# Optimization experiments

Measured on AMD Instinct MI355X. Metric: run time of the kernel, lower is better.

## Reference

```python
import jax, jax.numpy as jnp
import numpy as np

GRAVITY, MAIN_THRUST, SIDE_TORQUE, DT = 10.0, 6.0, 1.0, 0.02
H_OBS = jnp.array([[1, 0, 0, 0, 0, 0],
                   [0, 1, 0, 0, 0, 0],
                   [0, 0, 0, 0, 1, 0]], dtype=jnp.float32)  # (3,6)


def build_psd(log_diag, off_diag, dim):
    rows, cols = np.tril_indices(dim, -1)  # row-major, same order as torch.tril_indices
    L = jnp.zeros((dim, dim), dtype=log_diag.dtype)
    L = L.at[jnp.arange(dim), jnp.arange(dim)].set(jnp.exp(log_diag))
    L = L.at[rows, cols].set(off_diag)
    return L @ L.T + 1e-6 * jnp.eye(dim, dtype=log_diag.dtype)


def setup_inputs() -> dict:
    key = jax.random.key(0)
    B = 524288
    ks = jax.random.split(key, 8)
    z = jax.random.normal(ks[0], (B, 3), dtype=jnp.float32)
    u = jax.random.uniform(ks[1], (B, 2), dtype=jnp.float32)
    x_prev = jax.random.normal(ks[2], (B, 6), dtype=jnp.float32)
    A = 0.1 * jax.random.normal(ks[3], (B, 6, 6), dtype=jnp.float32)
    P_prev = jnp.einsum('bij,bkj->bik', A, A) + 0.5 * jnp.eye(6, dtype=jnp.float32)
    q_log_diag = jnp.array([-3.0, -3.0, -2.0, -2.0, -3.0, -2.0], dtype=jnp.float32)
    q_off_diag = 0.01 * jax.random.normal(ks[4], (15,), dtype=jnp.float32)
    r_log_diag = jnp.array([-2.0, -2.0, -2.0], dtype=jnp.float32)
    r_off_diag = 0.01 * jax.random.normal(ks[5], (3,), dtype=jnp.float32)
    return {"z": z, "u": u, "x_prev": x_prev, "P_prev": P_prev,
            "q_log_diag": q_log_diag, "q_off_diag": q_off_diag,
            "r_log_diag": r_log_diag, "r_off_diag": r_off_diag}


def _dynamics(x, u):
    px, py, vx, vy, theta, omega = (x[:, i] for i in range(6))
    main_power = jnp.clip(u[:, 0], 0.0, 1.0)
    lateral = u[:, 1]
    sin_th, cos_th = jnp.sin(theta), jnp.cos(theta)
    ax = -MAIN_THRUST * sin_th * main_power
    ay = MAIN_THRUST * cos_th * main_power - GRAVITY
    alpha = SIDE_TORQUE * lateral
    new_vx = vx + ax * DT
    new_vy = vy + ay * DT
    new_omega = omega + alpha * DT
    new_px = px + new_vx * DT
    new_py = py + new_vy * DT
    new_theta = theta + new_omega * DT
    return jnp.stack([new_px, new_py, new_vx, new_vy, new_theta, new_omega], axis=-1)


def _dynamics_jacobian(x, u):
    B = x.shape[0]
    theta = x[:, 4]
    main_power = jnp.clip(u[:, 0], 0.0, 1.0)
    sin_th, cos_th = jnp.sin(theta), jnp.cos(theta)
    Tm = MAIN_THRUST * main_power
    d = jnp.arange(6)
    F = jnp.zeros((B, 6, 6), dtype=x.dtype).at[:, d, d].set(1.0)
    F = F.at[:, 0, 2].set(DT).at[:, 1, 3].set(DT).at[:, 4, 5].set(DT)
    F = F.at[:, 2, 4].set(-Tm * cos_th * DT)
    F = F.at[:, 3, 4].set(-Tm * sin_th * DT)
    F = F.at[:, 0, 4].set(-Tm * cos_th * (DT * DT))
    F = F.at[:, 1, 4].set(-Tm * sin_th * (DT * DT))
    return F


def reference(z, u, x_prev, P_prev, q_log_diag, q_off_diag, r_log_diag, r_off_diag):
    Q = build_psd(q_log_diag, q_off_diag, 6)
    R = build_psd(r_log_diag, r_off_diag, 3)
    H = H_OBS
    # predict
    x_pred = _dynamics(x_prev, u)                              # (B,6)
    F = _dynamics_jacobian(x_prev, u)                          # (B,6,6)
    P_pred = jnp.einsum('bij,bjk,blk->bil', F, P_prev, F) + Q  # F P F^T + Q
    # update
    z_pred = jnp.einsum('ij,bj->bi', H, x_pred)                # (B,3)
    y = z - z_pred
    HP = jnp.einsum('ij,bjk->bik', H, P_pred)                  # (B,3,6)
    S = jnp.einsum('bij,kj->bik', HP, H) + R                   # (B,3,3)
    K = jnp.swapaxes(jnp.linalg.solve(S, HP), -1, -2)          # (B,6,3)
    x_upd = x_pred + jnp.einsum('bij,bj->bi', K, y)
    IKH = jnp.eye(6, dtype=x_pred.dtype) - jnp.einsum('bij,jk->bik', K, H)
    P_upd = (jnp.einsum('bij,bjk,blk->bil', IKH, P_pred, IKH)
             + jnp.einsum('bij,jk,blk->bil', K, R, K))          # Joseph form
    return (x_upd, P_upd)
```

## Files before the change

kernel.cpp:

```cpp
#include <hip/hip_runtime.h>

namespace {
constexpr float GRAVITY     = 10.0f;
constexpr float MAIN_THRUST = 6.0f;
constexpr float DT          = 0.02f;
}

__global__ __launch_bounds__(256) void ekf_kernel(
    const float* __restrict__ z,
    const float* __restrict__ u,
    const float* __restrict__ x_prev,
    const float* __restrict__ P_prev,
    const float* __restrict__ q_log_diag,
    const float* __restrict__ q_off_diag,
    const float* __restrict__ r_log_diag,
    const float* __restrict__ r_off_diag,
    float* __restrict__ x_out,
    float* __restrict__ P_out,
    int B)
{
    const int b = blockIdx.x * blockDim.x + threadIdx.x;
    if (b >= B) return;

    float L[6][6];
    #pragma unroll
    for (int i = 0; i < 6; ++i)
        #pragma unroll
        for (int j = 0; j < 6; ++j) L[i][j] = 0.0f;
    #pragma unroll
    for (int i = 0; i < 6; ++i) L[i][i] = expf(q_log_diag[i]);
    L[1][0] = q_off_diag[0];
    L[2][0] = q_off_diag[1];  L[2][1] = q_off_diag[2];
    L[3][0] = q_off_diag[3];  L[3][1] = q_off_diag[4];  L[3][2] = q_off_diag[5];
    L[4][0] = q_off_diag[6];  L[4][1] = q_off_diag[7];  L[4][2] = q_off_diag[8];
    L[4][3] = q_off_diag[9];
    L[5][0] = q_off_diag[10]; L[5][1] = q_off_diag[11]; L[5][2] = q_off_diag[12];
    L[5][3] = q_off_diag[13]; L[5][4] = q_off_diag[14];

    float Q[6][6];
    #pragma unroll
    for (int i = 0; i < 6; ++i) {
        #pragma unroll
        for (int j = 0; j <= i; ++j) {
            float s = 0.0f;
            #pragma unroll
            for (int k = 0; k <= j; ++k) s += L[i][k] * L[j][k];
            if (i == j) s += 1e-6f;
            Q[i][j] = s;
            Q[j][i] = s;
        }
    }

    float rd0 = expf(r_log_diag[0]);
    float rd1 = expf(r_log_diag[1]);
    float rd2 = expf(r_log_diag[2]);
    float ro0 = r_off_diag[0], ro1 = r_off_diag[1], ro2 = r_off_diag[2];
    float R00 = rd0 * rd0 + 1e-6f;
    float R10 = ro0 * rd0;
    float R11 = ro0 * ro0 + rd1 * rd1 + 1e-6f;
    float R20 = ro1 * rd0;
    float R21 = ro1 * ro0 + ro2 * rd1;
    float R22 = ro1 * ro1 + ro2 * ro2 + rd2 * rd2 + 1e-6f;
    float Rm[3][3] = {{R00, R10, R20}, {R10, R11, R21}, {R20, R21, R22}};

    const float2* xp2 = reinterpret_cast<const float2*>(x_prev + 6 * b);
    float2 x01 = xp2[0], x23 = xp2[1], x45 = xp2[2];
    const float px = x01.x, py = x01.y, vx = x23.x, vy = x23.y;
    const float th = x45.x, om = x45.y;

    const float2 uu = *reinterpret_cast<const float2*>(u + 2 * b);
    const float mp  = fminf(fmaxf(uu.x, 0.0f), 1.0f);
    const float lat = uu.y;

    float s_th, c_th;
    __sincosf(th, &s_th, &c_th);

    const float Tm  = MAIN_THRUST * mp;
    const float ax  = -Tm * s_th;
    const float ay  =  Tm * c_th - GRAVITY;
    const float nvx = vx + ax * DT;
    const float nvy = vy + ay * DT;
    const float nom = om + lat * DT;
    const float npx = px + nvx * DT;
    const float npy = py + nvy * DT;
    const float nth = th + nom * DT;
    float xp[6] = {npx, npy, nvx, nvy, nth, nom};

    const float f24 = -Tm * c_th * DT;
    const float f34 = -Tm * s_th * DT;
    const float f04 = f24 * DT;
    const float f14 = f34 * DT;

    float P[36];
    const float4* Pp4 = reinterpret_cast<const float4*>(P_prev + 36 * b);
    #pragma unroll
    for (int i = 0; i < 9; ++i) {
        float4 v = Pp4[i];
        P[4 * i + 0] = v.x; P[4 * i + 1] = v.y;
        P[4 * i + 2] = v.z; P[4 * i + 3] = v.w;
    }

    #pragma unroll
    for (int j = 0; j < 6; ++j) {
        P[0 * 6 + j] += DT * P[2 * 6 + j] + f04 * P[4 * 6 + j];
        P[1 * 6 + j] += DT * P[3 * 6 + j] + f14 * P[4 * 6 + j];
        P[2 * 6 + j] += f24 * P[4 * 6 + j];
        P[3 * 6 + j] += f34 * P[4 * 6 + j];
        P[4 * 6 + j] += DT * P[5 * 6 + j];
    }
    #pragma unroll
    for (int i = 0; i < 6; ++i) {
        const float m0 = P[i * 6 + 0], m1 = P[i * 6 + 1], m2 = P[i * 6 + 2];
        const float m3 = P[i * 6 + 3], m4 = P[i * 6 + 4], m5 = P[i * 6 + 5];
        P[i * 6 + 0] = m0 + DT * m2 + f04 * m4 + Q[i][0];
        P[i * 6 + 1] = m1 + DT * m3 + f14 * m4 + Q[i][1];
        P[i * 6 + 2] = m2 + f24 * m4 + Q[i][2];
        P[i * 6 + 3] = m3 + f34 * m4 + Q[i][3];
        P[i * 6 + 4] = m4 + DT * m5 + Q[i][4];
        P[i * 6 + 5] = m5 + Q[i][5];
    }

    const float* zp = z + 3 * b;
    const float y0 = zp[0] - npx;
    const float y1 = zp[1] - npy;
    const float y2 = zp[2] - nth;

    const float s00 = P[0 * 6 + 0] + Rm[0][0];
    const float s01 = P[0 * 6 + 1] + Rm[0][1];
    const float s02 = P[0 * 6 + 4] + Rm[0][2];
    const float s10 = P[1 * 6 + 0] + Rm[1][0];
    const float s11 = P[1 * 6 + 1] + Rm[1][1];
    const float s12 = P[1 * 6 + 4] + Rm[1][2];
    const float s20 = P[4 * 6 + 0] + Rm[2][0];
    const float s21 = P[4 * 6 + 1] + Rm[2][1];
    const float s22 = P[4 * 6 + 4] + Rm[2][2];

    const float det = s00 * (s11 * s22 - s12 * s21)
                    + s01 * (s12 * s20 - s10 * s22)
                    + s02 * (s10 * s21 - s11 * s20);
    const float invd = 1.0f / det;
    const float i00 = (s11 * s22 - s12 * s21) * invd;
    const float i01 = (s02 * s21 - s01 * s22) * invd;
    const float i02 = (s01 * s12 - s02 * s11) * invd;
    const float i10 = (s12 * s20 - s10 * s22) * invd;
    const float i11 = (s00 * s22 - s02 * s20) * invd;
    const float i12 = (s02 * s10 - s00 * s12) * invd;
    const float i20 = (s10 * s21 - s11 * s20) * invd;
    const float i21 = (s01 * s20 - s00 * s21) * invd;
    const float i22 = (s00 * s11 - s01 * s10) * invd;

    float K[6][3];
    #pragma unroll
    for (int i = 0; i < 6; ++i) {
        const float hp0 = P[0 * 6 + i];
        const float hp1 = P[1 * 6 + i];
        const float hp2 = P[4 * 6 + i];
        K[i][0] = i00 * hp0 + i01 * hp1 + i02 * hp2;
        K[i][1] = i10 * hp0 + i11 * hp1 + i12 * hp2;
        K[i][2] = i20 * hp0 + i21 * hp1 + i22 * hp2;
    }

    float2* xo2 = reinterpret_cast<float2*>(x_out + 6 * b);
    float xu[6];
    #pragma unroll
    for (int i = 0; i < 6; ++i)
        xu[i] = xp[i] + K[i][0] * y0 + K[i][1] * y1 + K[i][2] * y2;
    xo2[0] = make_float2(xu[0], xu[1]);
    xo2[1] = make_float2(xu[2], xu[3]);
    xo2[2] = make_float2(xu[4], xu[5]);

    float r0[6], r1[6], r4[6];
    #pragma unroll
    for (int j = 0; j < 6; ++j) {
        r0[j] = P[0 * 6 + j];
        r1[j] = P[1 * 6 + j];
        r4[j] = P[4 * 6 + j];
    }
    #pragma unroll
    for (int i = 0; i < 6; ++i)
        #pragma unroll
        for (int j = 0; j < 6; ++j)
            P[i * 6 + j] -= K[i][0] * r0[j] + K[i][1] * r1[j] + K[i][2] * r4[j];

    float c0[6], c1[6], c4[6];
    #pragma unroll
    for (int i = 0; i < 6; ++i) {
        c0[i] = P[i * 6 + 0];
        c1[i] = P[i * 6 + 1];
        c4[i] = P[i * 6 + 4];
    }
    float KR[6][3];
    #pragma unroll
    for (int i = 0; i < 6; ++i) {
        #pragma unroll
        for (int a = 0; a < 3; ++a)
            KR[i][a] = K[i][0] * Rm[0][a] + K[i][1] * Rm[1][a] + K[i][2] * Rm[2][a];
    }
    #pragma unroll
    for (int i = 0; i < 6; ++i) {
        #pragma unroll
        for (int j = 0; j < 6; ++j) {
            P[i * 6 + j] += -(c0[i] * K[j][0] + c1[i] * K[j][1] + c4[i] * K[j][2])
                            + (KR[i][0] * K[j][0] + KR[i][1] * K[j][1] + KR[i][2] * K[j][2]);
        }
    }

    float4* Po4 = reinterpret_cast<float4*>(P_out + 36 * b);
    #pragma unroll
    for (int i = 0; i < 9; ++i) {
        float4 v;
        v.x = P[4 * i + 0]; v.y = P[4 * i + 1];
        v.z = P[4 * i + 2]; v.w = P[4 * i + 3];
        Po4[i] = v;
    }
}

extern "C" void kernel_launch(void* const* d_in, const int* in_sizes, int n_in,
                              void* d_out, int out_size, void* d_ws, size_t ws_size,
                              hipStream_t stream) {
    const float* z          = (const float*)d_in[0];
    const float* u          = (const float*)d_in[1];
    const float* x_prev     = (const float*)d_in[2];
    const float* P_prev     = (const float*)d_in[3];
    const float* q_log_diag = (const float*)d_in[4];
    const float* q_off_diag = (const float*)d_in[5];
    const float* r_log_diag = (const float*)d_in[6];
    const float* r_off_diag = (const float*)d_in[7];

    const int B = in_sizes[0] / 3;
    float* x_out = (float*)d_out;
    float* P_out = (float*)d_out + (size_t)B * 6;

    const int block = 256;
    const int grid  = (B + block - 1) / block;
    ekf_kernel<<<grid, block, 0, stream>>>(z, u, x_prev, P_prev,
                                           q_log_diag, q_off_diag,
                                           r_log_diag, r_off_diag,
                                           x_out, P_out, B);
}
```

Before: 196.1 us.

## Stage P covariance loads and stores through padded shared memory for coalescing

Each block now loads its P_prev tile into shared memory with block-wide coalesced float4 reads, and threads read their own row from a stride-37 padded layout meant to avoid bank conflicts. After computing, each thread writes its result row back to shared memory, and the block writes P_out with coalesced float4 stores. This targets the strided per-thread 144-byte accesses of the old version. In exchange it adds about 37 KB of shared memory per block, which may limit occupancy, plus two barriers.

```diff
diff --git a/kernel.cpp b/kernel.cpp
--- a/kernel.cpp
+++ b/kernel.cpp
@@ -4,9 +4,11 @@
 constexpr float GRAVITY     = 10.0f;
 constexpr float MAIN_THRUST = 6.0f;
 constexpr float DT          = 0.02f;
+constexpr int   BLK         = 256;
+constexpr int   ROWPAD      = 37;
 }
 
-__global__ __launch_bounds__(256) void ekf_kernel(
+__global__ __launch_bounds__(BLK) void ekf_kernel(
     const float* __restrict__ z,
     const float* __restrict__ u,
     const float* __restrict__ x_prev,
@@ -19,199 +21,233 @@
     float* __restrict__ P_out,
     int B)
 {
-    const int b = blockIdx.x * blockDim.x + threadIdx.x;
-    if (b >= B) return;
-
-    float L[6][6];
-    #pragma unroll
-    for (int i = 0; i < 6; ++i)
-        #pragma unroll
-        for (int j = 0; j < 6; ++j) L[i][j] = 0.0f;
-    #pragma unroll
-    for (int i = 0; i < 6; ++i) L[i][i] = expf(q_log_diag[i]);
-    L[1][0] = q_off_diag[0];
-    L[2][0] = q_off_diag[1];  L[2][1] = q_off_diag[2];
-    L[3][0] = q_off_diag[3];  L[3][1] = q_off_diag[4];  L[3][2] = q_off_diag[5];
-    L[4][0] = q_off_diag[6];  L[4][1] = q_off_diag[7];  L[4][2] = q_off_diag[8];
-    L[4][3] = q_off_diag[9];
-    L[5][0] = q_off_diag[10]; L[5][1] = q_off_diag[11]; L[5][2] = q_off_diag[12];
-    L[5][3] = q_off_diag[13]; L[5][4] = q_off_diag[14];
-
-    float Q[6][6];
-    #pragma unroll
-    for (int i = 0; i < 6; ++i) {
-        #pragma unroll
-        for (int j = 0; j <= i; ++j) {
-            float s = 0.0f;
-            #pragma unroll
-            for (int k = 0; k <= j; ++k) s += L[i][k] * L[j][k];
-            if (i == j) s += 1e-6f;
-            Q[i][j] = s;
-            Q[j][i] = s;
+    __shared__ float smem[BLK * ROWPAD];
+
+    const int t = threadIdx.x;
+    const long long blockElem0 = (long long)blockIdx.x * BLK;
+    const long long elemsLeft  = (long long)B - blockElem0;
+    const int nElem  = elemsLeft >= BLK ? BLK : (int)elemsLeft;
+    const int count4 = nElem * 9;
+
+    {
+        const float4* gP4 = reinterpret_cast<const float4*>(P_prev + blockElem0 * 36);
+        #pragma unroll
+        for (int k = 0; k < 9; ++k) {
+            const int g4 = t + k * BLK;
+            if (g4 < count4) {
+                const float4 v = gP4[g4];
+                const int elem = g4 / 9;
+                const int off4 = g4 % 9;
+                float* dst = &smem[elem * ROWPAD + off4 * 4];
+                dst[0] = v.x; dst[1] = v.y; dst[2] = v.z; dst[3] = v.w;
+            }
         }
     }
-
-    float rd0 = expf(r_log_diag[0]);
-    float rd1 = expf(r_log_diag[1]);
-    float rd2 = expf(r_log_diag[2]);
-    float ro0 = r_off_diag[0], ro1 = r_off_diag[1], ro2 = r_off_diag[2];
-    float R00 = rd0 * rd0 + 1e-6f;
-    float R10 = ro0 * rd0;
-    float R11 = ro0 * ro0 + rd1 * rd1 + 1e-6f;
-    float R20 = ro1 * rd0;
-    float R21 = ro1 * ro0 + ro2 * rd1;
-    float R22 = ro1 * ro1 + ro2 * ro2 + rd2 * rd2 + 1e-6f;
-    float Rm[3][3] = {{R00, R10, R20}, {R10, R11, R21}, {R20, R21, R22}};
-
-    const float2* xp2 = reinterpret_cast<const float2*>(x_prev + 6 * b);
-    float2 x01 = xp2[0], x23 = xp2[1], x45 = xp2[2];
-    const float px = x01.x, py = x01.y, vx = x23.x, vy = x23.y;
-    const float th = x45.x, om = x45.y;
-
-    const float2 uu = *reinterpret_cast<const float2*>(u + 2 * b);
-    const float mp  = fminf(fmaxf(uu.x, 0.0f), 1.0f);
-    const float lat = uu.y;
-
-    float s_th, c_th;
-    __sincosf(th, &s_th, &c_th);
-
-    const float Tm  = MAIN_THRUST * mp;
-    const float ax  = -Tm * s_th;
-    const float ay  =  Tm * c_th - GRAVITY;
-    const float nvx = vx + ax * DT;
-    const float nvy = vy + ay * DT;
-    const float nom = om + lat * DT;
-    const float npx = px + nvx * DT;
-    const float npy = py + nvy * DT;
-    const float nth = th + nom * DT;
-    float xp[6] = {npx, npy, nvx, nvy, nth, nom};
-
-    const float f24 = -Tm * c_th * DT;
-    const float f34 = -Tm * s_th * DT;
-    const float f04 = f24 * DT;
-    const float f14 = f34 * DT;
-
-    float P[36];
-    const float4* Pp4 = reinterpret_cast<const float4*>(P_prev + 36 * b);
-    #pragma unroll
-    for (int i = 0; i < 9; ++i) {
-        float4 v = Pp4[i];
-        P[4 * i + 0] = v.x; P[4 * i + 1] = v.y;
-        P[4 * i + 2] = v.z; P[4 * i + 3] = v.w;
+    __syncthreads();
+
+    const bool valid = (t < nElem);
+    const long long b = blockElem0 + t;
+
+    if (valid) {
+        float L[6][6];
+        #pragma unroll
+        for (int i = 0; i < 6; ++i)
+            #pragma unroll
+            for (int j = 0; j < 6; ++j) L[i][j] = 0.0f;
+        #pragma unroll
+        for (int i = 0; i < 6; ++i) L[i][i] = expf(q_log_diag[i]);
+        L[1][0] = q_off_diag[0];
+        L[2][0] = q_off_diag[1];  L[2][1] = q_off_diag[2];
+        L[3][0] = q_off_diag[3];  L[3][1] = q_off_diag[4];  L[3][2] = q_off_diag[5];
+        L[4][0] = q_off_diag[6];  L[4][1] = q_off_diag[7];  L[4][2] = q_off_diag[8];
+        L[4][3] = q_off_diag[9];
+        L[5][0] = q_off_diag[10]; L[5][1] = q_off_diag[11]; L[5][2] = q_off_diag[12];
+        L[5][3] = q_off_diag[13]; L[5][4] = q_off_diag[14];
+
+        float Q[6][6];
+        #pragma unroll
+        for (int i = 0; i < 6; ++i) {
+            #pragma unroll
+            for (int j = 0; j <= i; ++j) {
+                float s = 0.0f;
+                #pragma unroll
+                for (int k = 0; k <= j; ++k) s += L[i][k] * L[j][k];
+                if (i == j) s += 1e-6f;
+                Q[i][j] = s;
+                Q[j][i] = s;
+            }
+        }
+
+        const float rd0 = expf(r_log_diag[0]);
+        const float rd1 = expf(r_log_diag[1]);
+        const float rd2 = expf(r_log_diag[2]);
+        const float ro0 = r_off_diag[0], ro1 = r_off_diag[1], ro2 = r_off_diag[2];
+        const float R00 = rd0 * rd0 + 1e-6f;
+        const float R10 = ro0 * rd0;
+        const float R11 = ro0 * ro0 + rd1 * rd1 + 1e-6f;
+        const float R20 = ro1 * rd0;
+        const float R21 = ro1 * ro0 + ro2 * rd1;
+        const float R22 = ro1 * ro1 + ro2 * ro2 + rd2 * rd2 + 1e-6f;
+        const float Rm[3][3] = {{R00, R10, R20}, {R10, R11, R21}, {R20, R21, R22}};
+
+        const float2* xp2 = reinterpret_cast<const float2*>(x_prev + 6 * b);
+        const float2 x01 = xp2[0], x23 = xp2[1], x45 = xp2[2];
+        const float px = x01.x, py = x01.y, vx = x23.x, vy = x23.y;
+        const float th = x45.x, om = x45.y;
+
+        const float2 uu = *reinterpret_cast<const float2*>(u + 2 * b);
+        const float mp  = fminf(fmaxf(uu.x, 0.0f), 1.0f);
+        const float lat = uu.y;
+
+        float s_th, c_th;
+        __sincosf(th, &s_th, &c_th);
+
+        const float Tm  = MAIN_THRUST * mp;
+        const float ax  = -Tm * s_th;
+        const float ay  =  Tm * c_th - GRAVITY;
+        const float nvx = vx + ax * DT;
+        const float nvy = vy + ay * DT;
+        const float nom = om + lat * DT;
+        const float npx = px + nvx * DT;
+        const float npy = py + nvy * DT;
+        const float nth = th + nom * DT;
+        const float xp[6] = {npx, npy, nvx, nvy, nth, nom};
+
+        const float f24 = -Tm * c_th * DT;
+        const float f34 = -Tm * s_th * DT;
+        const float f04 = f24 * DT;
+        const float f14 = f34 * DT;
+
+        float P[36];
+        const float* myrow = &smem[t * ROWPAD];
+        #pragma unroll
+        for (int j = 0; j < 36; ++j) P[j] = myrow[j];
+
+        #pragma unroll
+        for (int j = 0; j < 6; ++j) {
+            P[0 * 6 + j] += DT * P[2 * 6 + j] + f04 * P[4 * 6 + j];
+            P[1 * 6 + j] += DT * P[3 * 6 + j] + f14 * P[4 * 6 + j];
+            P[2 * 6 + j] += f24 * P[4 * 6 + j];
+            P[3 * 6 + j] += f34 * P[4 * 6 + j];
+            P[4 * 6 + j] += DT * P[5 * 6 + j];
+        }
+        #pragma unroll
+        for (int i = 0; i < 6; ++i) {
+            const float m0 = P[i * 6 + 0], m1 = P[i * 6 + 1], m2 = P[i * 6 + 2];
+            const float m3 = P[i * 6 + 3], m4 = P[i * 6 + 4], m5 = P[i * 6 + 5];
+            P[i * 6 + 0] = m0 + DT * m2 + f04 * m4 + Q[i][0];
+            P[i * 6 + 1] = m1 + DT * m3 + f14 * m4 + Q[i][1];
+            P[i * 6 + 2] = m2 + f24 * m4 + Q[i][2];
+            P[i * 6 + 3] = m3 + f34 * m4 + Q[i][3];
+            P[i * 6 + 4] = m4 + DT * m5 + Q[i][4];
+            P[i * 6 + 5] = m5 + Q[i][5];
+        }
+
+        const float* zp = z + 3 * b;
+        const float y0 = zp[0] - npx;
+        const float y1 = zp[1] - npy;
+        const float y2 = zp[2] - nth;
+
+        const float s00 = P[0 * 6 + 0] + Rm[0][0];
+        const float s01 = P[0 * 6 + 1] + Rm[0][1];
+        const float s02 = P[0 * 6 + 4] + Rm[0][2];
+        const float s10 = P[1 * 6 + 0] + Rm[1][0];
+        const float s11 = P[1 * 6 + 1] + Rm[1][1];
+        const float s12 = P[1 * 6 + 4] + Rm[1][2];
+        const float s20 = P[4 * 6 + 0] + Rm[2][0];
+        const float s21 = P[4 * 6 + 1] + Rm[2][1];
+        const float s22 = P[4 * 6 + 4] + Rm[2][2];
+
+        const float det = s00 * (s11 * s22 - s12 * s21)
+                        + s01 * (s12 * s20 - s10 * s22)
+                        + s02 * (s10 * s21 - s11 * s20);
+        const float invd = 1.0f / det;
+        const float i00 = (s11 * s22 - s12 * s21) * invd;
+        const float i01 = (s02 * s21 - s01 * s22) * invd;
+        const float i02 = (s01 * s12 - s02 * s11) * invd;
+        const float i10 = (s12 * s20 - s10 * s22) * invd;
+        const float i11 = (s00 * s22 - s02 * s20) * invd;
+        const float i12 = (s02 * s10 - s00 * s12) * invd;
+        const float i20 = (s10 * s21 - s11 * s20) * invd;
+        const float i21 = (s01 * s20 - s00 * s21) * invd;
+        const float i22 = (s00 * s11 - s01 * s10) * invd;
+
+        float K[6][3];
+        #pragma unroll
+        for (int i = 0; i < 6; ++i) {
+            const float hp0 = P[0 * 6 + i];
+            const float hp1 = P[1 * 6 + i];
+            const float hp2 = P[4 * 6 + i];
+            K[i][0] = i00 * hp0 + i01 * hp1 + i02 * hp2;
+            K[i][1] = i10 * hp0 + i11 * hp1 + i12 * hp2;
+            K[i][2] = i20 * hp0 + i21 * hp1 + i22 * hp2;
+        }
+
+        float2* xo2 = reinterpret_cast<float2*>(x_out + 6 * b);
+        float xu[6];
+        #pragma unroll
+        for (int i = 0; i < 6; ++i)
+            xu[i] = xp[i] + K[i][0] * y0 + K[i][1] * y1 + K[i][2] * y2;
+        xo2[0] = make_float2(xu[0], xu[1]);
+        xo2[1] = make_float2(xu[2], xu[3]);
+        xo2[2] = make_float2(xu[4], xu[5]);
+
+        float r0[6], r1[6], r4[6];
+        #pragma unroll
+        for (int j = 0; j < 6; ++j) {
+            r0[j] = P[0 * 6 + j];
+            r1[j] = P[1 * 6 + j];
+            r4[j] = P[4 * 6 + j];
+        }
+        #pragma unroll
+        for (int i = 0; i < 6; ++i)
+            #pragma unroll
+            for (int j = 0; j < 6; ++j)
+                P[i * 6 + j] -= K[i][0] * r0[j] + K[i][1] * r1[j] + K[i][2] * r4[j];
+
+        float c0[6], c1[6], c4[6];
+        #pragma unroll
+        for (int i = 0; i < 6; ++i) {
+            c0[i] = P[i * 6 + 0];
+            c1[i] = P[i * 6 + 1];
+            c4[i] = P[i * 6 + 4];
+        }
+        float KR[6][3];
+        #pragma unroll
+        for (int i = 0; i < 6; ++i) {
+            #pragma unroll
+            for (int a = 0; a < 3; ++a)
+                KR[i][a] = K[i][0] * Rm[0][a] + K[i][1] * Rm[1][a] + K[i][2] * Rm[2][a];
+        }
+        #pragma unroll
+        for (int i = 0; i < 6; ++i) {
+            #pragma unroll
+            for (int j = 0; j < 6; ++j) {
+                P[i * 6 + j] += -(c0[i] * K[j][0] + c1[i] * K[j][1] + c4[i] * K[j][2])
+                                + (KR[i][0] * K[j][0] + KR[i][1] * K[j][1] + KR[i][2] * K[j][2]);
+            }
+        }
+
+        float* myrowW = &smem[t * ROWPAD];
+        #pragma unroll
+        for (int j = 0; j < 36; ++j) myrowW[j] = P[j];
     }
-
-    #pragma unroll
-    for (int j = 0; j < 6; ++j) {
-        P[0 * 6 + j] += DT * P[2 * 6 + j] + f04 * P[4 * 6 + j];
-        P[1 * 6 + j] += DT * P[3 * 6 + j] + f14 * P[4 * 6 + j];
-        P[2 * 6 + j] += f24 * P[4 * 6 + j];
-        P[3 * 6 + j] += f34 * P[4 * 6 + j];
-        P[4 * 6 + j] += DT * P[5 * 6 + j];
-    }
-    #pragma unroll
-    for (int i = 0; i < 6; ++i) {
-        const float m0 = P[i * 6 + 0], m1 = P[i * 6 + 1], m2 = P[i * 6 + 2];
-        const float m3 = P[i * 6 + 3], m4 = P[i * 6 + 4], m5 = P[i * 6 + 5];
-        P[i * 6 + 0] = m0 + DT * m2 + f04 * m4 + Q[i][0];
-        P[i * 6 + 1] = m1 + DT * m3 + f14 * m4 + Q[i][1];
-        P[i * 6 + 2] = m2 + f24 * m4 + Q[i][2];
-        P[i * 6 + 3] = m3 + f34 * m4 + Q[i][3];
-        P[i * 6 + 4] = m4 + DT * m5 + Q[i][4];
-        P[i * 6 + 5] = m5 + Q[i][5];
-    }
-
-    const float* zp = z + 3 * b;
-    const float y0 = zp[0] - npx;
-    const float y1 = zp[1] - npy;
-    const float y2 = zp[2] - nth;
-
-    const float s00 = P[0 * 6 + 0] + Rm[0][0];
-    const float s01 = P[0 * 6 + 1] + Rm[0][1];
-    const float s02 = P[0 * 6 + 4] + Rm[0][2];
-    const float s10 = P[1 * 6 + 0] + Rm[1][0];
-    const float s11 = P[1 * 6 + 1] + Rm[1][1];
-    const float s12 = P[1 * 6 + 4] + Rm[1][2];
-    const float s20 = P[4 * 6 + 0] + Rm[2][0];
-    const float s21 = P[4 * 6 + 1] + Rm[2][1];
-    const float s22 = P[4 * 6 + 4] + Rm[2][2];
-
-    const float det = s00 * (s11 * s22 - s12 * s21)
-                    + s01 * (s12 * s20 - s10 * s22)
-                    + s02 * (s10 * s21 - s11 * s20);
-    const float invd = 1.0f / det;
-    const float i00 = (s11 * s22 - s12 * s21) * invd;
-    const float i01 = (s02 * s21 - s01 * s22) * invd;
-    const float i02 = (s01 * s12 - s02 * s11) * invd;
-    const float i10 = (s12 * s20 - s10 * s22) * invd;
-    const float i11 = (s00 * s22 - s02 * s20) * invd;
-    const float i12 = (s02 * s10 - s00 * s12) * invd;
-    const float i20 = (s10 * s21 - s11 * s20) * invd;
-    const float i21 = (s01 * s20 - s00 * s21) * invd;
-    const float i22 = (s00 * s11 - s01 * s10) * invd;
-
-    float K[6][3];
-    #pragma unroll
-    for (int i = 0; i < 6; ++i) {
-        const float hp0 = P[0 * 6 + i];
-        const float hp1 = P[1 * 6 + i];
-        const float hp2 = P[4 * 6 + i];
-        K[i][0] = i00 * hp0 + i01 * hp1 + i02 * hp2;
-        K[i][1] = i10 * hp0 + i11 * hp1 + i12 * hp2;
-        K[i][2] = i20 * hp0 + i21 * hp1 + i22 * hp2;
-    }
-
-    float2* xo2 = reinterpret_cast<float2*>(x_out + 6 * b);
-    float xu[6];
-    #pragma unroll
-    for (int i = 0; i < 6; ++i)
-        xu[i] = xp[i] + K[i][0] * y0 + K[i][1] * y1 + K[i][2] * y2;
-    xo2[0] = make_float2(xu[0], xu[1]);
-    xo2[1] = make_float2(xu[2], xu[3]);
-    xo2[2] = make_float2(xu[4], xu[5]);
-
-    float r0[6], r1[6], r4[6];
-    #pragma unroll
-    for (int j = 0; j < 6; ++j) {
-        r0[j] = P[0 * 6 + j];
-        r1[j] = P[1 * 6 + j];
-        r4[j] = P[4 * 6 + j];
-    }
-    #pragma unroll
-    for (int i = 0; i < 6; ++i)
-        #pragma unroll
-        for (int j = 0; j < 6; ++j)
-            P[i * 6 + j] -= K[i][0] * r0[j] + K[i][1] * r1[j] + K[i][2] * r4[j];
-
-    float c0[6], c1[6], c4[6];
-    #pragma unroll
-    for (int i = 0; i < 6; ++i) {
-        c0[i] = P[i * 6 + 0];
-        c1[i] = P[i * 6 + 1];
-        c4[i] = P[i * 6 + 4];
-    }
-    float KR[6][3];
-    #pragma unroll
-    for (int i = 0; i < 6; ++i) {
-        #pragma unroll
-        for (int a = 0; a < 3; ++a)
-            KR[i][a] = K[i][0] * Rm[0][a] + K[i][1] * Rm[1][a] + K[i][2] * Rm[2][a];
-    }
-    #pragma unroll
-    for (int i = 0; i < 6; ++i) {
-        #pragma unroll
-        for (int j = 0; j < 6; ++j) {
-            P[i * 6 + j] += -(c0[i] * K[j][0] + c1[i] * K[j][1] + c4[i] * K[j][2])
-                            + (KR[i][0] * K[j][0] + KR[i][1] * K[j][1] + KR[i][2] * K[j][2]);
-        }
-    }
-
-    float4* Po4 = reinterpret_cast<float4*>(P_out + 36 * b);
-    #pragma unroll
-    for (int i = 0; i < 9; ++i) {
-        float4 v;
-        v.x = P[4 * i + 0]; v.y = P[4 * i + 1];
-        v.z = P[4 * i + 2]; v.w = P[4 * i + 3];
-        Po4[i] = v;
+    __syncthreads();
+
+    {
+        float4* oP4 = reinterpret_cast<float4*>(P_out + blockElem0 * 36);
+        #pragma unroll
+        for (int k = 0; k < 9; ++k) {
+            const int g4 = t + k * BLK;
+            if (g4 < count4) {
+                const int elem = g4 / 9;
+                const int off4 = g4 % 9;
+                const float* src = &smem[elem * ROWPAD + off4 * 4];
+                float4 v;
+                v.x = src[0]; v.y = src[1]; v.z = src[2]; v.w = src[3];
+                oP4[g4] = v;
+            }
+        }
     }
 }
 
@@ -231,10 +267,9 @@
     float* x_out = (float*)d_out;
     float* P_out = (float*)d_out + (size_t)B * 6;
 
-    const int block = 256;
-    const int grid  = (B + block - 1) / block;
-    ekf_kernel<<<grid, block, 0, stream>>>(z, u, x_prev, P_prev,
-                                           q_log_diag, q_off_diag,
-                                           r_log_diag, r_off_diag,
-                                           x_out, P_out, B);
+    const int grid = (B + BLK - 1) / BLK;
+    ekf_kernel<<<grid, BLK, 0, stream>>>(z, u, x_prev, P_prev,
+                                         q_log_diag, q_off_diag,
+                                         r_log_diag, r_off_diag,
+                                         x_out, P_out, B);
 }
```

Result: faster. 191.7 us (-2.2%).
